# Kernel optimization log

Measured on AMD Instinct MI355X. Metric: run time of the kernel, lower is better.

The kernel has to match this reference:

```python
import jax, jax.numpy as jnp
import numpy as np

B, S, D, K, L, H = 2, 2048, 1024, 256, 2, 16
HD = D // H
F = 4 * D
EPS = 1e-5
NEG = -1e30


def setup_inputs() -> dict:
    key = jax.random.key(0)
    ks = jax.random.split(key, 20)
    # ragged segment boundaries: sorted, last boundary pinned to S-1 so the
    # expanded sequence is exactly seq_len long (required for torch.stack)
    boundaries = jnp.sort(jax.random.randint(ks[0], (B, K), 0, S - 1), axis=1)
    boundaries = boundaries.at[:, -1].set(S - 1).astype(jnp.int32)
    counts = jnp.full((B,), K, dtype=jnp.int32)
    x_processed = jax.random.normal(ks[1], (B, K, D), jnp.float32) * 0.02
    x_residual = jax.random.normal(ks[2], (B, S, D), jnp.float32) * 0.02
    # RoPE tables [S, HD]
    inv_freq = 1.0 / (10000.0 ** (jnp.arange(0, HD, 2, dtype=jnp.float32) / HD))
    freqs = jnp.outer(jnp.arange(S, dtype=jnp.float32), inv_freq)
    emb = jnp.concatenate([freqs, freqs], axis=-1)
    cos, sin = jnp.cos(emb), jnp.sin(emb)
    sc = D ** -0.5
    params = dict(
        start_emb=jax.random.normal(ks[3], (D,), jnp.float32) * 0.02,
        Wq=jax.random.normal(ks[4], (L, D, D)) * sc,
        Wk=jax.random.normal(ks[5], (L, D, D)) * sc,
        Wv=jax.random.normal(ks[6], (L, D, D)) * sc,
        Wo=jax.random.normal(ks[7], (L, D, D)) * sc,
        Wg=jax.random.normal(ks[8], (L, D, F)) * sc,
        Wu=jax.random.normal(ks[9], (L, D, F)) * sc,
        Wd=jax.random.normal(ks[10], (L, F, D)) * (F ** -0.5),
        ln1=jnp.ones((L, D), jnp.float32),
        ln2=jnp.ones((L, D), jnp.float32),
        fnorm=jnp.ones((D,), jnp.float32),
    )
    return dict(x_processed=x_processed, boundaries=boundaries, counts=counts,
                x_residual=x_residual, cos=cos, sin=sin, seq_len=S, **params)


def _rms(x, w):
    return x * jax.lax.rsqrt(jnp.mean(x * x, axis=-1, keepdims=True) + EPS) * w


def _rope(x, cos, sin):
    # x: [B, H, S, HD]; cos/sin: [S, HD]
    x1, x2 = jnp.split(x, 2, axis=-1)
    rot = jnp.concatenate([-x2, x1], axis=-1)
    return x * cos[None, None] + rot * sin[None, None]


def reference(x_processed, boundaries, counts, x_residual, cos, sin, seq_len,
              start_emb, Wq, Wk, Wv, Wo, Wg, Wu, Wd, ln1, ln2, fnorm):
    b, k, d = x_processed.shape
    # --- vectorized ragged repeat-expand ---
    # position t belongs to segment i iff boundaries[i-1] < t <= boundaries[i]
    t = jnp.arange(seq_len)
    valid = jnp.arange(k)[None, :] < counts[:, None]
    bnd = jnp.where(valid, boundaries, seq_len)          # mask out unused slots
    seg = jax.vmap(lambda bb: jnp.searchsorted(bb, t, side='left'))(bnd)  # [B,S]
    # segment 0 -> start_emb, segment i>0 -> x_processed[:, i-1]
    reps = jnp.concatenate(
        [jnp.broadcast_to(start_emb, (b, 1, d)), x_processed], axis=1)  # [B,K+1,D]
    x = jnp.take_along_axis(reps, seg[..., None], axis=1) + x_residual

    causal = jnp.tril(jnp.ones((seq_len, seq_len), bool))
    scale = HD ** -0.5
    for l in range(L):
        h = _rms(x, ln1[l])
        q = (h @ Wq[l]).reshape(b, seq_len, H, HD).transpose(0, 2, 1, 3)
        kk = (h @ Wk[l]).reshape(b, seq_len, H, HD).transpose(0, 2, 1, 3)
        v = (h @ Wv[l]).reshape(b, seq_len, H, HD).transpose(0, 2, 1, 3)
        q, kk = _rope(q, cos, sin), _rope(kk, cos, sin)
        att = jnp.einsum('bhqd,bhkd->bhqk', q, kk) * scale
        att = jax.nn.softmax(jnp.where(causal, att, NEG), axis=-1)
        o = jnp.einsum('bhqk,bhkd->bhqd', att, v)
        o = o.transpose(0, 2, 1, 3).reshape(b, seq_len, d)
        x = x + o @ Wo[l]
        h = _rms(x, ln2[l])
        x = x + (jax.nn.silu(h @ Wg[l]) * (h @ Wu[l])) @ Wd[l]
    return _rms(x, fnorm)
```

## Files before the change

### kernel.cpp

```cpp
#include <hip/hip_runtime.h>
#include <hip/hip_bf16.h>

#define S_LEN  2048
#define NB     2
#define DIM    1024
#define KSEG   256
#define NLAYER 2
#define NHEAD  16
#define HDIM   64
#define FDIM   4096
#define NROW   (NB * S_LEN)

typedef __bf16 bf16x8 __attribute__((ext_vector_type(8)));
typedef float  f32x4  __attribute__((ext_vector_type(4)));
typedef __hip_bfloat16 bf16_t;

struct __align__(8)  us4 { unsigned short v[4]; };
struct __align__(16) us8 { unsigned short v[8]; };

__device__ __forceinline__ unsigned short f2bf(float f) {
  __hip_bfloat16 t = __float2bfloat16(f);
  return __builtin_bit_cast(unsigned short, t);
}
__device__ __forceinline__ float bf2f(unsigned short x) {
  return __bfloat162float(__builtin_bit_cast(__hip_bfloat16, x));
}

__device__ __forceinline__ void gload_lds16(const void* g, void* l) {
  __builtin_amdgcn_global_load_lds((__attribute__((address_space(1))) void*)g,
                                   (__attribute__((address_space(3))) void*)l,
                                   16, 0, 0);
}

__device__ __forceinline__ f32x4 mfma16(bf16x8 a, bf16x8 b, f32x4 c) {
  return __builtin_amdgcn_mfma_f32_16x16x32_bf16(a, b, c, 0, 0, 0);
}

__device__ __forceinline__ bf16_t* swz(bf16_t* base, int r, int kElem) {
  int byte = ((r << 7) + (kElem << 1)) ^ ((r & 7) << 4);
  return (bf16_t*)((char*)base + byte);
}
__device__ __forceinline__ const bf16_t* swz(const bf16_t* base, int r, int kElem) {
  int byte = ((r << 7) + (kElem << 1)) ^ ((r & 7) << 4);
  return (const bf16_t*)((const char*)base + byte);
}

__global__ __launch_bounds__(256) void expand_kernel(
    const float* __restrict__ xp, const int* __restrict__ bnd,
    const int* __restrict__ counts, const float* __restrict__ xres,
    const float* __restrict__ semb, float* __restrict__ x) {
  const int bt = blockIdx.x;
  const int b = bt >> 11, t = bt & (S_LEN - 1);
  const int cnt = counts[b];
  const int* bb = bnd + b * KSEG;
  int lo = 0, hi = KSEG;
  while (lo < hi) {
    int mid = (lo + hi) >> 1;
    int v = (mid < cnt) ? bb[mid] : S_LEN;
    if (v < t) lo = mid + 1; else hi = mid;
  }
  const float* src = (lo == 0) ? semb : (xp + ((size_t)b * KSEG + (lo - 1)) * DIM);
  const int tid = threadIdx.x;
  float4 a = ((const float4*)src)[tid];
  float4 r = ((const float4*)(xres + (size_t)bt * DIM))[tid];
  float4 w; w.x = a.x + r.x; w.y = a.y + r.y; w.z = a.z + r.z; w.w = a.w + r.w;
  ((float4*)(x + (size_t)bt * DIM))[tid] = w;
}

template <int F32OUT>
__global__ __launch_bounds__(256) void rmsnorm_kernel(
    const float* __restrict__ x, const float* __restrict__ wgt,
    bf16_t* __restrict__ ob, float* __restrict__ of) {
  const int row = blockIdx.x, tid = threadIdx.x;
  const float4 v = ((const float4*)(x + (size_t)row * DIM))[tid];
  float ss = v.x * v.x + v.y * v.y + v.z * v.z + v.w * v.w;
#pragma unroll
  for (int off = 1; off < 64; off <<= 1) ss += __shfl_xor(ss, off);
  __shared__ float red[4];
  if ((tid & 63) == 0) red[tid >> 6] = ss;
  __syncthreads();
  ss = red[0] + red[1] + red[2] + red[3];
  const float r = rsqrtf(ss * (1.0f / DIM) + 1e-5f);
  const float4 wv = ((const float4*)wgt)[tid];
  if (F32OUT) {
    float4 o4; o4.x = v.x * r * wv.x; o4.y = v.y * r * wv.y;
    o4.z = v.z * r * wv.z; o4.w = v.w * r * wv.w;
    ((float4*)(of + (size_t)row * DIM))[tid] = o4;
  } else {
    us4 p;
    p.v[0] = f2bf(v.x * r * wv.x); p.v[1] = f2bf(v.y * r * wv.y);
    p.v[2] = f2bf(v.z * r * wv.z); p.v[3] = f2bf(v.w * r * wv.w);
    ((us4*)(ob + (size_t)row * DIM))[tid] = p;
  }
}

template <int MODE>
__global__ __launch_bounds__(256) void transpose_cast(
    const float* __restrict__ in, bf16_t* __restrict__ out, int R, int C) {
  __shared__ float tile[32][33];
  const int tx = threadIdx.x & 31, ty = threadIdx.x >> 5;
  const int cb = blockIdx.x * 32, rb = blockIdx.y * 32;
#pragma unroll
  for (int i = 0; i < 4; i++) {
    int r = ty + i * 8;
    tile[r][tx] = in[(size_t)(rb + r) * C + cb + tx];
  }
  __syncthreads();
#pragma unroll
  for (int i = 0; i < 4; i++) {
    int r = ty + i * 8;
    int n = cb + r;
    int dr = (MODE == 0) ? n : (((n >> 4) << 5) + (n & 15) + (MODE == 2 ? 16 : 0));
    out[(size_t)dr * R + rb + tx] = __float2bfloat16(tile[tx][r]);
  }
}

template <int FUSE>
__global__ __launch_bounds__(512, 2) void gemm_bt256(
    const bf16_t* __restrict__ A, const bf16_t* __restrict__ Bt,
    bf16_t* __restrict__ C, int ldc, int K, int lda, int nbn, int nbm,
    const float* __restrict__ cosb, const float* __restrict__ sinb) {
  __shared__ __align__(16) bf16_t As[2][256][64];
  __shared__ __align__(16) bf16_t Bs[2][256][64];
  const int bid = blockIdx.x;
  const int bmC = nbm >> 1, bnC = nbn >> 2;
  const int c8 = bid & 7, idx = bid >> 3;
  const int bm = (c8 & 1) * bmC + idx / bnC;
  const int bn = (c8 >> 1) * bnC + idx % bnC;
  const int tid = threadIdx.x;
  const int lane = tid & 63, w = tid >> 6;
  const int wm = w >> 2, wn = w & 3;
  const int l15 = lane & 15, l16 = lane >> 4;
  const bf16_t* Ag = A + (size_t)bm * 256 * lda;
  const bf16_t* Bg = Bt + (size_t)bn * 256 * K;
  const int NT = K >> 6;

  f32x4 acc[8][4] = {};

  auto stage = [&](int j) {
    const int t = j >> 2, item = j & 3, buf = t & 1;
    bf16_t* dst;
    const bf16_t* src;
    int stride;
    if (item < 2) { dst = &Bs[buf][item * 128][0];
                    src = Bg + (size_t)item * 128 * K;  stride = K;   }
    else          { dst = &As[buf][(item - 2) * 128][0];
                    src = Ag + (size_t)(item - 2) * 128 * lda; stride = lda; }
    const int k0 = t << 6;
#pragma unroll
    for (int i = 0; i < 2; i++) {
      int c = i * 512 + tid;
      int row = c >> 3, q = c & 7;
      int colE = (q ^ (row & 7)) << 3;
      gload_lds16(src + (size_t)row * stride + k0 + colE, dst + c * 8);
    }
  };
  auto frag = [&](const bf16_t* tile, int row, int kk) -> bf16x8 {
    int byte = ((row << 7) + (kk << 6) + (l16 << 4)) ^ ((row & 7) << 4);
    return *(const bf16x8*)((const char*)tile + byte);
  };

  for (int j = 0; j < 7; j++) stage(j);
  asm volatile("s_waitcnt vmcnt(6)" ::: "memory");
  __builtin_amdgcn_s_barrier();

  for (int t = 0; t < NT; t++) {
    const int buf = t & 1;
    const bf16_t* At = &As[buf][0][0];
    const bf16_t* Bc = &Bs[buf][0][0];
    bf16x8 bfrg[4][2];
    const int jb = (t << 2) + 7;
#pragma unroll
    for (int p = 0; p < 4; p++) {
      bf16x8 afrg[2][2];
      if (p == 0) {
#pragma unroll
        for (int ni = 0; ni < 4; ni++)
#pragma unroll
          for (int kk = 0; kk < 2; kk++)
            bfrg[ni][kk] = frag(Bc, wn * 64 + ni * 16 + l15, kk);
      }
#pragma unroll
      for (int mi = 0; mi < 2; mi++)
#pragma unroll
        for (int kk = 0; kk < 2; kk++)
          afrg[mi][kk] = frag(At, wm * 128 + p * 32 + mi * 16 + l15, kk);
      if (jb + p < 4 * NT) stage(jb + p);
      __builtin_amdgcn_sched_barrier(0);
      __builtin_amdgcn_s_barrier();
      asm volatile("s_waitcnt lgkmcnt(0)" ::: "memory");
      __builtin_amdgcn_sched_barrier(0);
      __builtin_amdgcn_s_setprio(1);
#pragma unroll
      for (int mi = 0; mi < 2; mi++)
#pragma unroll
        for (int ni = 0; ni < 4; ni++)
#pragma unroll
          for (int kk = 0; kk < 2; kk++)
            acc[p * 2 + mi][ni] = mfma16(afrg[mi][kk], bfrg[ni][kk],
                                         acc[p * 2 + mi][ni]);
      __builtin_amdgcn_s_setprio(0);
      __builtin_amdgcn_sched_barrier(0);
      if (p == 3) {
        if (t < NT - 2) { asm volatile("s_waitcnt vmcnt(6)" ::: "memory"); }
        else            { asm volatile("s_waitcnt vmcnt(0)" ::: "memory"); }
      }
      __builtin_amdgcn_s_barrier();
    }
  }

  const int r0 = bm * 256 + wm * 128 + (l16 << 2);
  if (FUSE == 0) {
    const int c0 = bn * 256 + wn * 64 + l15;
#pragma unroll
    for (int mi = 0; mi < 8; mi++)
#pragma unroll
      for (int ni = 0; ni < 4; ni++)
#pragma unroll
        for (int r = 0; r < 4; r++)
          C[(size_t)(r0 + mi * 16 + r) * ldc + c0 + ni * 16] =
              __float2bfloat16(acc[mi][ni][r]);
  } else if (FUSE == 1) {
    const int c0 = bn * 128 + wn * 32 + l15;
#pragma unroll
    for (int mi = 0; mi < 8; mi++)
#pragma unroll
      for (int j = 0; j < 2; j++)
#pragma unroll
        for (int r = 0; r < 4; r++) {
          float g = acc[mi][2 * j][r], u = acc[mi][2 * j + 1][r];
          float a = g / (1.f + __expf(-g)) * u;
          C[(size_t)(r0 + mi * 16 + r) * ldc + c0 + j * 16] = __float2bfloat16(a);
        }
  } else {
    const int c0 = bn * 256 + wn * 64 + l15;
    if (bn < 8) {
#pragma unroll
      for (int mi = 0; mi < 8; mi++)
#pragma unroll
        for (int r = 0; r < 4; r++) {
          const int row = r0 + mi * 16 + r;
          const int tt = row & (S_LEN - 1);
#pragma unroll
          for (int ni = 0; ni < 2; ni++) {
            const int i = ni * 16 + l15;
            const float cz = cosb[tt * HDIM + i];
            const float sz = sinb[tt * HDIM + i];
            const float x1 = acc[mi][ni][r], x2 = acc[mi][ni + 2][r];
            C[(size_t)row * ldc + c0 + ni * 16] =
                __float2bfloat16(x1 * cz - x2 * sz);
            C[(size_t)row * ldc + c0 + (ni + 2) * 16] =
                __float2bfloat16(x2 * cz + x1 * sz);
          }
        }
    } else {
#pragma unroll
      for (int mi = 0; mi < 8; mi++)
#pragma unroll
        for (int ni = 0; ni < 4; ni++)
#pragma unroll
          for (int r = 0; r < 4; r++)
            C[(size_t)(r0 + mi * 16 + r) * ldc + c0 + ni * 16] =
                __float2bfloat16(acc[mi][ni][r]);
    }
  }
}

template <int EPI>
__global__ __launch_bounds__(256) void gemm_sn(
    const bf16_t* __restrict__ A, const bf16_t* __restrict__ Bt,
    bf16_t* __restrict__ Cb, float* __restrict__ Cf, int N, int K, int lda) {
  __shared__ __align__(16) bf16_t As[3][128][64];
  __shared__ __align__(16) bf16_t Bs[3][64][64];
  const int nbn = N >> 6;
  const int bid = blockIdx.x;
  const int sbid = (bid & 7) * (gridDim.x >> 3) + (bid >> 3);
  const int bn = sbid % nbn, bm = sbid / nbn;
  const int tid = threadIdx.x, lane = tid & 63, w = tid >> 6;
  const int wm = w >> 1, wn = w & 1;
  const int l15 = lane & 15, l16 = lane >> 4;
  const bf16_t* Ag = A + (size_t)bm * 128 * lda;
  const bf16_t* Bg = Bt + (size_t)bn * 64 * K;
  f32x4 acc[4][2] = {};
  const int NT = K >> 6;

  auto stage = [&](int buf, int t) {
    const int k0 = t << 6;
#pragma unroll
    for (int i = 0; i < 4; i++) {
      int c = i * 256 + tid;
      int row = c >> 3, q = c & 7;
      int colE = (q ^ (row & 7)) << 3;
      gload_lds16(Ag + (size_t)row * lda + k0 + colE, &As[buf][0][0] + c * 8);
    }
#pragma unroll
    for (int i = 0; i < 2; i++) {
      int c = i * 256 + tid;
      int row = c >> 3, q = c & 7;
      int colE = (q ^ (row & 7)) << 3;
      gload_lds16(Bg + (size_t)row * K + k0 + colE, &Bs[buf][0][0] + c * 8);
    }
  };
  auto frag = [&](const bf16_t* base, int row, int kk) -> bf16x8 {
    int byte = ((row << 7) + (kk << 6) + (l16 << 4)) ^ ((row & 7) << 4);
    return *(const bf16x8*)((const char*)base + byte);
  };

  stage(0, 0);
  if (NT > 1) stage(1, 1);
  int bi = 0;
  for (int t = 0; t < NT; t++) {
    if (t + 1 < NT) { asm volatile("s_waitcnt vmcnt(6)" ::: "memory"); }
    else            { asm volatile("s_waitcnt vmcnt(0)" ::: "memory"); }
    __builtin_amdgcn_s_barrier();
    __builtin_amdgcn_sched_barrier(0);
    if (t + 2 < NT) {
      int nb = bi + 2; if (nb >= 3) nb -= 3;
      stage(nb, t + 2);
    }
    __builtin_amdgcn_sched_barrier(0);
    const bf16_t* Ab = &As[bi][0][0];
    const bf16_t* Bb = &Bs[bi][0][0];
    bf16x8 af[4][2], bfr[2][2];
#pragma unroll
    for (int mi = 0; mi < 4; mi++)
#pragma unroll
      for (int kk = 0; kk < 2; kk++)
        af[mi][kk] = frag(Ab, wm * 64 + mi * 16 + l15, kk);
#pragma unroll
    for (int ni = 0; ni < 2; ni++)
#pragma unroll
      for (int kk = 0; kk < 2; kk++)
        bfr[ni][kk] = frag(Bb, wn * 32 + ni * 16 + l15, kk);
    __builtin_amdgcn_s_setprio(1);
#pragma unroll
    for (int mi = 0; mi < 4; mi++)
#pragma unroll
      for (int ni = 0; ni < 2; ni++)
#pragma unroll
        for (int kk = 0; kk < 2; kk++)
          acc[mi][ni] = mfma16(af[mi][kk], bfr[ni][kk], acc[mi][ni]);
    __builtin_amdgcn_s_setprio(0);
    __builtin_amdgcn_sched_barrier(0);
    bi++; if (bi >= 3) bi -= 3;
  }

  const int r0 = bm * 128 + wm * 64 + (l16 << 2);
  const int c0 = bn * 64 + wn * 32 + l15;
#pragma unroll
  for (int mi = 0; mi < 4; mi++)
#pragma unroll
    for (int ni = 0; ni < 2; ni++)
#pragma unroll
      for (int r = 0; r < 4; r++) {
        size_t off = (size_t)(r0 + mi * 16 + r) * N + c0 + ni * 16;
        if (EPI == 0) Cb[off] = __float2bfloat16(acc[mi][ni][r]);
        else          Cf[off] += acc[mi][ni][r];
      }
}

__global__ __launch_bounds__(256) void vtrans_kernel(
    const bf16_t* __restrict__ qkv, bf16_t* __restrict__ vT) {
  const int gid = blockIdx.x;
  const int tb = gid & 31, bh = gid >> 5;
  const int b = bh >> 4, h = bh & 15;
  __shared__ bf16_t tile[64][65];
  const int tx = threadIdx.x, ty = threadIdx.y;
  const bf16_t* src = qkv + ((size_t)(b * S_LEN + tb * 64)) * 3072 + 2048 + h * HDIM;
#pragma unroll
  for (int j = 0; j < 16; j++)
    tile[j * 4 + ty][tx] = src[(size_t)(j * 4 + ty) * 3072 + tx];
  __syncthreads();
  bf16_t* dst = vT + ((size_t)bh * 64) * S_LEN + tb * 64;
#pragma unroll
  for (int j = 0; j < 16; j++) {
    int d = j * 4 + ty;
    dst[(size_t)d * S_LEN + tx] = tile[tx][d];
  }
}

__global__ __launch_bounds__(256) void attn_kernel(
    const bf16_t* __restrict__ qkv, const bf16_t* __restrict__ vT,
    bf16_t* __restrict__ o) {
  __shared__ __align__(16) bf16_t Ks[3][64][64];
  __shared__ __align__(16) bf16_t Vs[3][64][64];
  __shared__ __align__(16) bf16_t Ps[64][64];
  const int bid = blockIdx.x;
  const int pair = (bid >> 3) & 15;
  const int bh = (bid & 7) + ((bid >> 7) << 3);
  const int b = bh >> 4, h = bh & 15;
  const int tid = threadIdx.x, lane = tid & 63, w = tid >> 6;
  const int l15 = lane & 15;
  const int kq = (lane >> 4) << 3;
  const int rq = (lane >> 4) << 2;
  const bf16_t* kbase = qkv + (size_t)b * S_LEN * 3072 + 1024 + h * HDIM;
  const bf16_t* vbase = vT + ((size_t)bh * 64) * S_LEN;

  bf16x8 ones;
#pragma unroll
  for (int e = 0; e < 8; e++) ones[e] = (__bf16)1.0f;

#define STAGE(buf, kt) do {                                                    \
    const bf16_t* kg_ = kbase + (size_t)(kt) * 64 * 3072;                      \
    const bf16_t* vg_ = vbase + (kt) * 64;                                     \
    _Pragma("unroll")                                                          \
    for (int i_ = 0; i_ < 2; i_++) {                                           \
      int cb_ = i_ * 256 + w * 64;                                             \
      int c_ = cb_ + lane;                                                     \
      int row_ = c_ >> 3;                                                      \
      int colE_ = ((c_ & 7) ^ (row_ & 7)) << 3;                                \
      gload_lds16(kg_ + (size_t)row_ * 3072 + colE_,                           \
                  &Ks[buf][0][0] + (size_t)cb_ * 8);                           \
      gload_lds16(vg_ + (size_t)row_ * S_LEN + colE_,                          \
                  &Vs[buf][0][0] + (size_t)cb_ * 8);                           \
    }                                                                          \
  } while (0)

  for (int ph = 0; ph < 2; ph++) {
    const int qb = (ph == 0) ? pair : (31 - pair);
    const int nk = qb + 1;
    const int qrow = qb * 64 + w * 16 + l15;
    const bf16_t* qg = qkv + ((size_t)(b * S_LEN + qrow)) * 3072 + h * HDIM;
    bf16x8 aq0 = *(const bf16x8*)(qg + kq);
    bf16x8 aq1 = *(const bf16x8*)(qg + 32 + kq);
    const float qsc = 0.125f * 1.44269504088896340736f;
#pragma unroll
    for (int e = 0; e < 8; e++) {
      aq0[e] = (__bf16)((float)aq0[e] * qsc);
      aq1[e] = (__bf16)((float)aq1[e] * qsc);
    }
    f32x4 oacc[4] = {};
    f32x4 lacc = {0.f, 0.f, 0.f, 0.f};
    float m_s = -1e30f;
    const int myq = qb * 64 + w * 16 + l15;

    __builtin_amdgcn_s_barrier();
    STAGE(0, 0);
    if (nk > 1) STAGE(1, 1);
    int bi = 0;
    for (int kt = 0; kt < nk; kt++) {
      if (kt + 1 < nk) { asm volatile("s_waitcnt vmcnt(4)" ::: "memory"); }
      else             { asm volatile("s_waitcnt vmcnt(0)" ::: "memory"); }
      __builtin_amdgcn_s_barrier();
      __builtin_amdgcn_sched_barrier(0);
      if (kt + 2 < nk) {
        int nb = bi + 2; if (nb >= 3) nb -= 3;
        STAGE(nb, kt + 2);
      }
      __builtin_amdgcn_sched_barrier(0);
      const bf16_t* Kc = &Ks[bi][0][0];
      const bf16_t* Vc = &Vs[bi][0][0];
      f32x4 st[4];
      __builtin_amdgcn_s_setprio(1);
#pragma unroll
      for (int f = 0; f < 4; f++) {
        bf16x8 bk0 = *(const bf16x8*)swz(Kc, f * 16 + l15, kq);
        bf16x8 bk1 = *(const bf16x8*)swz(Kc, f * 16 + l15, 32 + kq);
        f32x4 t = {};
        t = mfma16(bk0, aq0, t);
        t = mfma16(bk1, aq1, t);
        st[f] = t;
      }
      __builtin_amdgcn_s_setprio(0);
      if (kt == qb) {
#pragma unroll
        for (int f = 0; f < 4; f++) {
          int kvb = kt * 64 + f * 16 + rq;
#pragma unroll
          for (int r = 0; r < 4; r++)
            if (kvb + r > myq) st[f][r] = -1e30f;
        }
      }
      float mx = -1e30f;
#pragma unroll
      for (int f = 0; f < 4; f++)
#pragma unroll
        for (int r = 0; r < 4; r++) mx = fmaxf(mx, st[f][r]);
      mx = fmaxf(mx, __shfl_xor(mx, 16));
      mx = fmaxf(mx, __shfl_xor(mx, 32));
      const float mn = fmaxf(m_s, mx);
      const float alpha = exp2f(m_s - mn);
      m_s = mn;
#pragma unroll
      for (int f = 0; f < 4; f++)
#pragma unroll
        for (int r = 0; r < 4; r++) st[f][r] = exp2f(st[f][r] - mn);
      float alpr[4];
#pragma unroll
      for (int r = 0; r < 4; r++) alpr[r] = __shfl(alpha, rq + r);
#pragma unroll
      for (int ni = 0; ni < 4; ni++)
#pragma unroll
        for (int r = 0; r < 4; r++) oacc[ni][r] *= alpr[r];
#pragma unroll
      for (int r = 0; r < 4; r++) lacc[r] *= alpr[r];
#pragma unroll
      for (int f = 0; f < 4; f++) {
        us4 pk;
#pragma unroll
        for (int r = 0; r < 4; r++) pk.v[r] = f2bf(st[f][r]);
        *(us4*)swz(&Ps[0][0], w * 16 + l15, f * 16 + rq) = pk;
      }
      __builtin_amdgcn_s_setprio(1);
#pragma unroll
      for (int kk2 = 0; kk2 < 2; kk2++) {
        bf16x8 ap = *(const bf16x8*)swz(&Ps[0][0], w * 16 + l15, kk2 * 32 + kq);
        lacc = mfma16(ap, ones, lacc);
#pragma unroll
        for (int ni = 0; ni < 4; ni++) {
          bf16x8 bv = *(const bf16x8*)swz(Vc, ni * 16 + l15, kk2 * 32 + kq);
          oacc[ni] = mfma16(ap, bv, oacc[ni]);
        }
      }
      __builtin_amdgcn_s_setprio(0);
      __builtin_amdgcn_sched_barrier(0);
      bi++; if (bi >= 3) bi -= 3;
    }
    bf16_t* ob = o + ((size_t)(b * S_LEN + qb * 64 + w * 16 + rq)) * DIM + h * HDIM + l15;
#pragma unroll
    for (int r = 0; r < 4; r++) {
      float inv = 1.0f / lacc[r];
#pragma unroll
      for (int ni = 0; ni < 4; ni++)
        ob[(size_t)r * DIM + ni * 16] = __float2bfloat16(oacc[ni][r] * inv);
    }
  }
#undef STAGE
}

extern "C" void kernel_launch(void* const* d_in, const int* in_sizes, int n_in,
                              void* d_out, int out_size, void* d_ws, size_t ws_size,
                              hipStream_t stream) {
  (void)in_sizes; (void)n_in; (void)out_size; (void)ws_size;
  const float* x_processed = (const float*)d_in[0];
  const int*   boundaries  = (const int*)d_in[1];
  const int*   counts      = (const int*)d_in[2];
  const float* x_residual  = (const float*)d_in[3];
  const float* cos_t       = (const float*)d_in[4];
  const float* sin_t       = (const float*)d_in[5];
  const float* start_emb   = (const float*)d_in[7];
  const float* Wq  = (const float*)d_in[8];
  const float* Wk  = (const float*)d_in[9];
  const float* Wv  = (const float*)d_in[10];
  const float* Wo  = (const float*)d_in[11];
  const float* Wg  = (const float*)d_in[12];
  const float* Wu  = (const float*)d_in[13];
  const float* Wd  = (const float*)d_in[14];
  const float* ln1 = (const float*)d_in[15];
  const float* ln2 = (const float*)d_in[16];
  const float* fnm = (const float*)d_in[17];

  char* ws = (char*)d_ws;
  const size_t MB = (size_t)1 << 20;
  float*  x      = (float*)(ws);
  bf16_t* h      = (bf16_t*)(ws + 16 * MB);
  bf16_t* Wqkv_t = (bf16_t*)(ws + 24 * MB);
  bf16_t* Wo_t   = (bf16_t*)(ws + 30 * MB);
  bf16_t* Wgu_t  = (bf16_t*)(ws + 32 * MB);
  bf16_t* Wd_t   = (bf16_t*)(ws + 48 * MB);
  char*   Rg     = ws + 56 * MB;
  bf16_t* qkv  = (bf16_t*)(Rg);
  bf16_t* vT   = (bf16_t*)(Rg + 24 * MB);
  bf16_t* obuf = (bf16_t*)(Rg + 32 * MB);
  bf16_t* act  = (bf16_t*)(Rg);

  expand_kernel<<<NROW, 256, 0, stream>>>(x_processed, boundaries, counts,
                                          x_residual, start_emb, x);

  const size_t dd = (size_t)DIM * DIM, df = (size_t)DIM * FDIM;
  for (int l = 0; l < NLAYER; l++) {
    transpose_cast<0><<<dim3(DIM / 32, DIM / 32), 256, 0, stream>>>(Wq + l * dd, Wqkv_t, DIM, DIM);
    transpose_cast<0><<<dim3(DIM / 32, DIM / 32), 256, 0, stream>>>(Wk + l * dd, Wqkv_t + dd, DIM, DIM);
    transpose_cast<0><<<dim3(DIM / 32, DIM / 32), 256, 0, stream>>>(Wv + l * dd, Wqkv_t + 2 * dd, DIM, DIM);
    transpose_cast<0><<<dim3(DIM / 32, DIM / 32), 256, 0, stream>>>(Wo + l * dd, Wo_t, DIM, DIM);
    transpose_cast<1><<<dim3(FDIM / 32, DIM / 32), 256, 0, stream>>>(Wg + l * df, Wgu_t, DIM, FDIM);
    transpose_cast<2><<<dim3(FDIM / 32, DIM / 32), 256, 0, stream>>>(Wu + l * df, Wgu_t, DIM, FDIM);
    transpose_cast<0><<<dim3(DIM / 32, FDIM / 32), 256, 0, stream>>>(Wd + l * df, Wd_t, FDIM, DIM);

    rmsnorm_kernel<0><<<NROW, 256, 0, stream>>>(x, ln1 + l * DIM, h, nullptr);
    gemm_bt256<2><<<(3072 / 256) * (NROW / 256), 512, 0, stream>>>(
        h, Wqkv_t, qkv, 3072, DIM, DIM, 3072 / 256, NROW / 256, cos_t, sin_t);
    vtrans_kernel<<<NB * NHEAD * (S_LEN / 64), dim3(64, 4), 0, stream>>>(qkv, vT);
    attn_kernel<<<512, 256, 0, stream>>>(qkv, vT, obuf);
    gemm_sn<1><<<(DIM / 64) * (NROW / 128), 256, 0, stream>>>(
        obuf, Wo_t, nullptr, x, DIM, DIM, DIM);

    rmsnorm_kernel<0><<<NROW, 256, 0, stream>>>(x, ln2 + l * DIM, h, nullptr);
    gemm_bt256<1><<<(2 * FDIM / 256) * (NROW / 256), 512, 0, stream>>>(
        h, Wgu_t, act, FDIM, DIM, DIM, 2 * FDIM / 256, NROW / 256, nullptr, nullptr);
    gemm_sn<1><<<(DIM / 64) * (NROW / 128), 256, 0, stream>>>(
        act, Wd_t, nullptr, x, DIM, FDIM, FDIM);
  }
  rmsnorm_kernel<1><<<NROW, 256, 0, stream>>>(x, fnm, nullptr, (float*)d_out);
}
```

Measured before the change: 589.9 us.

## Use 128-row query tiles per block in attention, replacing paired-tile scheduling

```diff
diff --git a/kernel.cpp b/kernel.cpp
--- a/kernel.cpp
+++ b/kernel.cpp
@@ -384,10 +384,11 @@
     bf16_t* __restrict__ o) {
   __shared__ __align__(16) bf16_t Ks[3][64][64];
   __shared__ __align__(16) bf16_t Vs[3][64][64];
-  __shared__ __align__(16) bf16_t Ps[64][64];
+  __shared__ __align__(16) bf16_t Ps[128][64];
   const int bid = blockIdx.x;
-  const int pair = (bid >> 3) & 15;
-  const int bh = (bid & 7) + ((bid >> 7) << 3);
+  const int idx = bid >> 3;
+  const int bh = ((idx >> 4) << 3) + (bid & 7);
+  const int qb = 15 - (idx & 15);
   const int b = bh >> 4, h = bh & 15;
   const int tid = threadIdx.x, lane = tid & 63, w = tid >> 6;
   const int l15 = lane & 15;
@@ -416,113 +417,133 @@
     }                                                                          \
   } while (0)
 
-  for (int ph = 0; ph < 2; ph++) {
-    const int qb = (ph == 0) ? pair : (31 - pair);
-    const int nk = qb + 1;
-    const int qrow = qb * 64 + w * 16 + l15;
-    const bf16_t* qg = qkv + ((size_t)(b * S_LEN + qrow)) * 3072 + h * HDIM;
-    bf16x8 aq0 = *(const bf16x8*)(qg + kq);
-    bf16x8 aq1 = *(const bf16x8*)(qg + 32 + kq);
-    const float qsc = 0.125f * 1.44269504088896340736f;
+  const int nk = 2 * qb + 2;
+  const int q0 = qb * 128 + w * 32;
+  const float qsc = 0.125f * 1.44269504088896340736f;
+  bf16x8 aq[2][2];
+  int myq[2];
+#pragma unroll
+  for (int qg = 0; qg < 2; qg++) {
+    const int qrow = q0 + qg * 16 + l15;
+    myq[qg] = qrow;
+    const bf16_t* qg_p = qkv + ((size_t)(b * S_LEN + qrow)) * 3072 + h * HDIM;
+    aq[qg][0] = *(const bf16x8*)(qg_p + kq);
+    aq[qg][1] = *(const bf16x8*)(qg_p + 32 + kq);
 #pragma unroll
     for (int e = 0; e < 8; e++) {
-      aq0[e] = (__bf16)((float)aq0[e] * qsc);
-      aq1[e] = (__bf16)((float)aq1[e] * qsc);
-    }
-    f32x4 oacc[4] = {};
-    f32x4 lacc = {0.f, 0.f, 0.f, 0.f};
-    float m_s = -1e30f;
-    const int myq = qb * 64 + w * 16 + l15;
-
+      aq[qg][0][e] = (__bf16)((float)aq[qg][0][e] * qsc);
+      aq[qg][1][e] = (__bf16)((float)aq[qg][1][e] * qsc);
+    }
+  }
+  f32x4 oacc[2][4] = {};
+  f32x4 lacc[2] = {};
+  float m_s[2] = {-1e30f, -1e30f};
+
+  STAGE(0, 0);
+  STAGE(1, 1);
+  int bi = 0;
+  for (int kt = 0; kt < nk; kt++) {
+    if (kt + 1 < nk) { asm volatile("s_waitcnt vmcnt(4)" ::: "memory"); }
+    else             { asm volatile("s_waitcnt vmcnt(0)" ::: "memory"); }
     __builtin_amdgcn_s_barrier();
-    STAGE(0, 0);
-    if (nk > 1) STAGE(1, 1);
-    int bi = 0;
-    for (int kt = 0; kt < nk; kt++) {
-      if (kt + 1 < nk) { asm volatile("s_waitcnt vmcnt(4)" ::: "memory"); }
-      else             { asm volatile("s_waitcnt vmcnt(0)" ::: "memory"); }
-      __builtin_amdgcn_s_barrier();
-      __builtin_amdgcn_sched_barrier(0);
-      if (kt + 2 < nk) {
-        int nb = bi + 2; if (nb >= 3) nb -= 3;
-        STAGE(nb, kt + 2);
+    __builtin_amdgcn_sched_barrier(0);
+    if (kt + 2 < nk) {
+      int nb = bi + 2; if (nb >= 3) nb -= 3;
+      STAGE(nb, kt + 2);
+    }
+    __builtin_amdgcn_sched_barrier(0);
+    const bf16_t* Kc = &Ks[bi][0][0];
+    const bf16_t* Vc = &Vs[bi][0][0];
+    f32x4 st[2][4];
+    __builtin_amdgcn_s_setprio(1);
+#pragma unroll
+    for (int f = 0; f < 4; f++) {
+      bf16x8 bk0 = *(const bf16x8*)swz(Kc, f * 16 + l15, kq);
+      bf16x8 bk1 = *(const bf16x8*)swz(Kc, f * 16 + l15, 32 + kq);
+#pragma unroll
+      for (int qg = 0; qg < 2; qg++) {
+        f32x4 t = {};
+        t = mfma16(bk0, aq[qg][0], t);
+        t = mfma16(bk1, aq[qg][1], t);
+        st[qg][f] = t;
       }
-      __builtin_amdgcn_sched_barrier(0);
-      const bf16_t* Kc = &Ks[bi][0][0];
-      const bf16_t* Vc = &Vs[bi][0][0];
-      f32x4 st[4];
-      __builtin_amdgcn_s_setprio(1);
-#pragma unroll
-      for (int f = 0; f < 4; f++) {
-        bf16x8 bk0 = *(const bf16x8*)swz(Kc, f * 16 + l15, kq);
-        bf16x8 bk1 = *(const bf16x8*)swz(Kc, f * 16 + l15, 32 + kq);
-        f32x4 t = {};
-        t = mfma16(bk0, aq0, t);
-        t = mfma16(bk1, aq1, t);
-        st[f] = t;
-      }
-      __builtin_amdgcn_s_setprio(0);
-      if (kt == qb) {
+    }
+    __builtin_amdgcn_s_setprio(0);
+    if (kt >= 2 * qb) {
+#pragma unroll
+      for (int qg = 0; qg < 2; qg++)
 #pragma unroll
         for (int f = 0; f < 4; f++) {
           int kvb = kt * 64 + f * 16 + rq;
 #pragma unroll
           for (int r = 0; r < 4; r++)
-            if (kvb + r > myq) st[f][r] = -1e30f;
+            if (kvb + r > myq[qg]) st[qg][f][r] = -1e30f;
         }
-      }
+    }
+#pragma unroll
+    for (int qg = 0; qg < 2; qg++) {
       float mx = -1e30f;
 #pragma unroll
       for (int f = 0; f < 4; f++)
 #pragma unroll
-        for (int r = 0; r < 4; r++) mx = fmaxf(mx, st[f][r]);
+        for (int r = 0; r < 4; r++) mx = fmaxf(mx, st[qg][f][r]);
       mx = fmaxf(mx, __shfl_xor(mx, 16));
       mx = fmaxf(mx, __shfl_xor(mx, 32));
-      const float mn = fmaxf(m_s, mx);
-      const float alpha = exp2f(m_s - mn);
-      m_s = mn;
+      const float mn = fmaxf(m_s[qg], mx);
+      const float alpha = exp2f(m_s[qg] - mn);
+      m_s[qg] = mn;
 #pragma unroll
       for (int f = 0; f < 4; f++)
 #pragma unroll
-        for (int r = 0; r < 4; r++) st[f][r] = exp2f(st[f][r] - mn);
+        for (int r = 0; r < 4; r++) st[qg][f][r] = exp2f(st[qg][f][r] - mn);
       float alpr[4];
 #pragma unroll
       for (int r = 0; r < 4; r++) alpr[r] = __shfl(alpha, rq + r);
 #pragma unroll
       for (int ni = 0; ni < 4; ni++)
 #pragma unroll
-        for (int r = 0; r < 4; r++) oacc[ni][r] *= alpr[r];
-#pragma unroll
-      for (int r = 0; r < 4; r++) lacc[r] *= alpr[r];
+        for (int r = 0; r < 4; r++) oacc[qg][ni][r] *= alpr[r];
+#pragma unroll
+      for (int r = 0; r < 4; r++) lacc[qg][r] *= alpr[r];
 #pragma unroll
       for (int f = 0; f < 4; f++) {
         us4 pk;
 #pragma unroll
-        for (int r = 0; r < 4; r++) pk.v[r] = f2bf(st[f][r]);
-        *(us4*)swz(&Ps[0][0], w * 16 + l15, f * 16 + rq) = pk;
+        for (int r = 0; r < 4; r++) pk.v[r] = f2bf(st[qg][f][r]);
+        *(us4*)swz(&Ps[0][0], w * 32 + qg * 16 + l15, f * 16 + rq) = pk;
       }
-      __builtin_amdgcn_s_setprio(1);
-#pragma unroll
-      for (int kk2 = 0; kk2 < 2; kk2++) {
-        bf16x8 ap = *(const bf16x8*)swz(&Ps[0][0], w * 16 + l15, kk2 * 32 + kq);
-        lacc = mfma16(ap, ones, lacc);
-#pragma unroll
-        for (int ni = 0; ni < 4; ni++) {
-          bf16x8 bv = *(const bf16x8*)swz(Vc, ni * 16 + l15, kk2 * 32 + kq);
-          oacc[ni] = mfma16(ap, bv, oacc[ni]);
-        }
+    }
+    __builtin_amdgcn_s_setprio(1);
+#pragma unroll
+    for (int kk2 = 0; kk2 < 2; kk2++) {
+      bf16x8 ap[2];
+#pragma unroll
+      for (int qg = 0; qg < 2; qg++) {
+        ap[qg] = *(const bf16x8*)swz(&Ps[0][0], w * 32 + qg * 16 + l15,
+                                     kk2 * 32 + kq);
+        lacc[qg] = mfma16(ap[qg], ones, lacc[qg]);
       }
-      __builtin_amdgcn_s_setprio(0);
-      __builtin_amdgcn_sched_barrier(0);
-      bi++; if (bi >= 3) bi -= 3;
-    }
-    bf16_t* ob = o + ((size_t)(b * S_LEN + qb * 64 + w * 16 + rq)) * DIM + h * HDIM + l15;
+#pragma unroll
+      for (int ni = 0; ni < 4; ni++) {
+        bf16x8 bv = *(const bf16x8*)swz(Vc, ni * 16 + l15, kk2 * 32 + kq);
+#pragma unroll
+        for (int qg = 0; qg < 2; qg++)
+          oacc[qg][ni] = mfma16(ap[qg], bv, oacc[qg][ni]);
+      }
+    }
+    __builtin_amdgcn_s_setprio(0);
+    __builtin_amdgcn_sched_barrier(0);
+    bi++; if (bi >= 3) bi -= 3;
+  }
+#pragma unroll
+  for (int qg = 0; qg < 2; qg++) {
+    bf16_t* ob = o + ((size_t)(b * S_LEN + q0 + qg * 16 + rq)) * DIM + h * HDIM + l15;
 #pragma unroll
     for (int r = 0; r < 4; r++) {
-      float inv = 1.0f / lacc[r];
+      float inv = 1.0f / lacc[qg][r];
 #pragma unroll
       for (int ni = 0; ni < 4; ni++)
-        ob[(size_t)r * DIM + ni * 16] = __float2bfloat16(oacc[ni][r] * inv);
+        ob[(size_t)r * DIM + ni * 16] = __float2bfloat16(oacc[qg][ni][r] * inv);
     }
   }
 #undef STAGE
```

After: 644.1 us. 9.2% more time.

## Fuse V transpose into QKV GEMM epilogue and drop LDS staging in attention

Applied to the files above, without the earlier changes.

```diff
diff --git a/kernel.cpp b/kernel.cpp
--- a/kernel.cpp
+++ b/kernel.cpp
@@ -119,7 +119,8 @@
 __global__ __launch_bounds__(512, 2) void gemm_bt256(
     const bf16_t* __restrict__ A, const bf16_t* __restrict__ Bt,
     bf16_t* __restrict__ C, int ldc, int K, int lda, int nbn, int nbm,
-    const float* __restrict__ cosb, const float* __restrict__ sinb) {
+    const float* __restrict__ cosb, const float* __restrict__ sinb,
+    bf16_t* __restrict__ vTout) {
   __shared__ __align__(16) bf16_t As[2][256][64];
   __shared__ __align__(16) bf16_t Bs[2][256][64];
   const int bid = blockIdx.x;
@@ -254,14 +255,18 @@
           }
         }
     } else {
+      const int hh = (bn - 8) * 4 + wn;
+      const int b = r0 >> 11, t0 = r0 & (S_LEN - 1);
 #pragma unroll
       for (int mi = 0; mi < 8; mi++)
 #pragma unroll
-        for (int ni = 0; ni < 4; ni++)
-#pragma unroll
-          for (int r = 0; r < 4; r++)
-            C[(size_t)(r0 + mi * 16 + r) * ldc + c0 + ni * 16] =
-                __float2bfloat16(acc[mi][ni][r]);
+        for (int ni = 0; ni < 4; ni++) {
+          us4 pk;
+#pragma unroll
+          for (int r = 0; r < 4; r++) pk.v[r] = f2bf(acc[mi][ni][r]);
+          *(us4*)&vTout[((size_t)((b << 4) + hh) * 64 + ni * 16 + l15) * S_LEN
+                        + t0 + mi * 16] = pk;
+        }
     }
   }
 }
@@ -359,31 +364,9 @@
       }
 }
 
-__global__ __launch_bounds__(256) void vtrans_kernel(
-    const bf16_t* __restrict__ qkv, bf16_t* __restrict__ vT) {
-  const int gid = blockIdx.x;
-  const int tb = gid & 31, bh = gid >> 5;
-  const int b = bh >> 4, h = bh & 15;
-  __shared__ bf16_t tile[64][65];
-  const int tx = threadIdx.x, ty = threadIdx.y;
-  const bf16_t* src = qkv + ((size_t)(b * S_LEN + tb * 64)) * 3072 + 2048 + h * HDIM;
-#pragma unroll
-  for (int j = 0; j < 16; j++)
-    tile[j * 4 + ty][tx] = src[(size_t)(j * 4 + ty) * 3072 + tx];
-  __syncthreads();
-  bf16_t* dst = vT + ((size_t)bh * 64) * S_LEN + tb * 64;
-#pragma unroll
-  for (int j = 0; j < 16; j++) {
-    int d = j * 4 + ty;
-    dst[(size_t)d * S_LEN + tx] = tile[tx][d];
-  }
-}
-
 __global__ __launch_bounds__(256) void attn_kernel(
     const bf16_t* __restrict__ qkv, const bf16_t* __restrict__ vT,
     bf16_t* __restrict__ o) {
-  __shared__ __align__(16) bf16_t Ks[3][64][64];
-  __shared__ __align__(16) bf16_t Vs[3][64][64];
   __shared__ __align__(16) bf16_t Ps[64][64];
   const int bid = blockIdx.x;
   const int pair = (bid >> 3) & 15;
@@ -400,22 +383,6 @@
 #pragma unroll
   for (int e = 0; e < 8; e++) ones[e] = (__bf16)1.0f;
 
-#define STAGE(buf, kt) do {                                                    \
-    const bf16_t* kg_ = kbase + (size_t)(kt) * 64 * 3072;                      \
-    const bf16_t* vg_ = vbase + (kt) * 64;                                     \
-    _Pragma("unroll")                                                          \
-    for (int i_ = 0; i_ < 2; i_++) {                                           \
-      int cb_ = i_ * 256 + w * 64;                                             \
-      int c_ = cb_ + lane;                                                     \
-      int row_ = c_ >> 3;                                                      \
-      int colE_ = ((c_ & 7) ^ (row_ & 7)) << 3;                                \
-      gload_lds16(kg_ + (size_t)row_ * 3072 + colE_,                           \
-                  &Ks[buf][0][0] + (size_t)cb_ * 8);                           \
-      gload_lds16(vg_ + (size_t)row_ * S_LEN + colE_,                          \
-                  &Vs[buf][0][0] + (size_t)cb_ * 8);                           \
-    }                                                                          \
-  } while (0)
-
   for (int ph = 0; ph < 2; ph++) {
     const int qb = (ph == 0) ? pair : (31 - pair);
     const int nk = qb + 1;
@@ -434,28 +401,14 @@
     float m_s = -1e30f;
     const int myq = qb * 64 + w * 16 + l15;
 
-    __builtin_amdgcn_s_barrier();
-    STAGE(0, 0);
-    if (nk > 1) STAGE(1, 1);
-    int bi = 0;
     for (int kt = 0; kt < nk; kt++) {
-      if (kt + 1 < nk) { asm volatile("s_waitcnt vmcnt(4)" ::: "memory"); }
-      else             { asm volatile("s_waitcnt vmcnt(0)" ::: "memory"); }
-      __builtin_amdgcn_s_barrier();
-      __builtin_amdgcn_sched_barrier(0);
-      if (kt + 2 < nk) {
-        int nb = bi + 2; if (nb >= 3) nb -= 3;
-        STAGE(nb, kt + 2);
-      }
-      __builtin_amdgcn_sched_barrier(0);
-      const bf16_t* Kc = &Ks[bi][0][0];
-      const bf16_t* Vc = &Vs[bi][0][0];
       f32x4 st[4];
       __builtin_amdgcn_s_setprio(1);
 #pragma unroll
       for (int f = 0; f < 4; f++) {
-        bf16x8 bk0 = *(const bf16x8*)swz(Kc, f * 16 + l15, kq);
-        bf16x8 bk1 = *(const bf16x8*)swz(Kc, f * 16 + l15, 32 + kq);
+        const bf16_t* kr = kbase + (size_t)(kt * 64 + f * 16 + l15) * 3072;
+        bf16x8 bk0 = *(const bf16x8*)(kr + kq);
+        bf16x8 bk1 = *(const bf16x8*)(kr + 32 + kq);
         f32x4 t = {};
         t = mfma16(bk0, aq0, t);
         t = mfma16(bk1, aq1, t);
@@ -508,13 +461,12 @@
         lacc = mfma16(ap, ones, lacc);
 #pragma unroll
         for (int ni = 0; ni < 4; ni++) {
-          bf16x8 bv = *(const bf16x8*)swz(Vc, ni * 16 + l15, kk2 * 32 + kq);
+          bf16x8 bv = *(const bf16x8*)(vbase + (size_t)(ni * 16 + l15) * S_LEN
+                                       + kt * 64 + kk2 * 32 + kq);
           oacc[ni] = mfma16(ap, bv, oacc[ni]);
         }
       }
       __builtin_amdgcn_s_setprio(0);
-      __builtin_amdgcn_sched_barrier(0);
-      bi++; if (bi >= 3) bi -= 3;
     }
     bf16_t* ob = o + ((size_t)(b * S_LEN + qb * 64 + w * 16 + rq)) * DIM + h * HDIM + l15;
 #pragma unroll
@@ -525,7 +477,6 @@
         ob[(size_t)r * DIM + ni * 16] = __float2bfloat16(oacc[ni][r] * inv);
     }
   }
-#undef STAGE
 }
 
 extern "C" void kernel_launch(void* const* d_in, const int* in_sizes, int n_in,
@@ -579,15 +530,15 @@
 
     rmsnorm_kernel<0><<<NROW, 256, 0, stream>>>(x, ln1 + l * DIM, h, nullptr);
     gemm_bt256<2><<<(3072 / 256) * (NROW / 256), 512, 0, stream>>>(
-        h, Wqkv_t, qkv, 3072, DIM, DIM, 3072 / 256, NROW / 256, cos_t, sin_t);
-    vtrans_kernel<<<NB * NHEAD * (S_LEN / 64), dim3(64, 4), 0, stream>>>(qkv, vT);
+        h, Wqkv_t, qkv, 3072, DIM, DIM, 3072 / 256, NROW / 256, cos_t, sin_t, vT);
     attn_kernel<<<512, 256, 0, stream>>>(qkv, vT, obuf);
     gemm_sn<1><<<(DIM / 64) * (NROW / 128), 256, 0, stream>>>(
         obuf, Wo_t, nullptr, x, DIM, DIM, DIM);
 
     rmsnorm_kernel<0><<<NROW, 256, 0, stream>>>(x, ln2 + l * DIM, h, nullptr);
     gemm_bt256<1><<<(2 * FDIM / 256) * (NROW / 256), 512, 0, stream>>>(
-        h, Wgu_t, act, FDIM, DIM, DIM, 2 * FDIM / 256, NROW / 256, nullptr, nullptr);
+        h, Wgu_t, act, FDIM, DIM, DIM, 2 * FDIM / 256, NROW / 256,
+        nullptr, nullptr, nullptr);
     gemm_sn<1><<<(DIM / 64) * (NROW / 128), 256, 0, stream>>>(
         act, Wd_t, nullptr, x, DIM, FDIM, FDIM);
   }
```

Result: slower. 723.9 us (+22.7%).
